# Performance work log

Measured on AMD Instinct MI355X. Metric: run time of the kernel, lower is better.

## Reference

```python
import jax, jax.numpy as jnp
import numpy as np

N_HEAD = 16


def _rope_tables(T, head_dim, dtype):
    # RotaryEmbedding buffers: freqs = outer(t, inv_freq), half-dim tables [T, head_dim//2]
    inv_freq = 1.0 / (10000.0 ** (jnp.arange(0, head_dim, 2, dtype=jnp.float32) / head_dim))
    freqs = jnp.arange(T, dtype=jnp.float32)[:, None] * inv_freq[None, :]
    return jnp.cos(freqs).astype(dtype), jnp.sin(freqs).astype(dtype)


def _apply_rotary(x, cos, sin):
    # x: [B,H,T,D]; cos/sin: [T,D//2] broadcast over B,H
    d = x.shape[-1] // 2
    x1, x2 = x[..., :d], x[..., d:]
    return jnp.concatenate([x1 * cos - x2 * sin, x2 * cos + x1 * sin], axis=-1)


def setup_inputs() -> dict:
    key = jax.random.key(0)
    k1, k2, k3 = jax.random.split(key, 3)
    B, T, C = 2, 2048, 2048
    x = jax.random.normal(k1, (B, T, C), dtype=jnp.float32)
    Wqkv = jax.random.normal(k2, (C, 3 * C), dtype=jnp.float32) * (1.0 / np.sqrt(C))
    Wproj = jax.random.normal(k3, (C, C), dtype=jnp.float32) * (1.0 / np.sqrt(C))
    return {"x": x, "Wqkv": Wqkv, "Wproj": Wproj}


def reference(x, Wqkv, Wproj):
    B, T, C = x.shape
    H = N_HEAD
    D = C // H
    qkv = (x @ Wqkv).reshape(B, T, 3, H, D)
    q, k, v = qkv[:, :, 0], qkv[:, :, 1], qkv[:, :, 2]  # [B,T,H,D]
    q = jnp.transpose(q, (0, 2, 1, 3))  # [B,H,T,D]
    k = jnp.transpose(k, (0, 2, 1, 3))
    v = jnp.transpose(v, (0, 2, 1, 3))
    cos, sin = _rope_tables(T, D, x.dtype)
    q = _apply_rotary(q, cos, sin)
    k = _apply_rotary(k, cos, sin)
    scale = 1.0 / np.sqrt(D)
    scores = jnp.einsum('bhqd,bhkd->bhqk', q, k) * scale
    causal = jnp.tril(jnp.ones((T, T), dtype=bool))
    scores = jnp.where(causal, scores, jnp.finfo(scores.dtype).min)
    attn = jax.nn.softmax(scores, axis=-1)
    out = jnp.einsum('bhqk,bhkd->bhqd', attn, v)
    out = jnp.transpose(out, (0, 2, 1, 3)).reshape(B, T, C)
    return out @ Wproj
```

## Files before the change

### kernel.cpp

```cpp
#include <hip/hip_runtime.h>
#include <hip/hip_bf16.h>

typedef short s16b;
using bf16x4 = __attribute__((ext_vector_type(4))) short;
using bf16x8 = __attribute__((ext_vector_type(8))) short;
using f32x4  = __attribute__((ext_vector_type(4))) float;
using u32x4  = __attribute__((ext_vector_type(4))) unsigned;

#define DEVINL __device__ __forceinline__

DEVINL float bf2f(short u) {
    union { float f; unsigned u; } x;
    x.u = ((unsigned)(unsigned short)u) << 16;
    return x.f;
}
DEVINL short f2bf(float f) {
    unsigned u = __builtin_bit_cast(unsigned, f);
    u += 0x7FFFu + ((u >> 16) & 1u);
    return (short)(u >> 16);
}
DEVINL unsigned cvtpk(float a, float b) {
    unsigned r;
    asm("v_cvt_pk_bf16_f32 %0, %1, %2" : "=v"(r) : "v"(a), "v"(b));
    return r;
}

DEVINL f32x4 mfma16(bf16x8 a, bf16x8 b, f32x4 c) {
    return __builtin_amdgcn_mfma_f32_16x16x32_bf16(a, b, c, 0, 0, 0);
}

DEVINL void gload_lds16(const void* g, void* lds_uniform) {
    __builtin_amdgcn_global_load_lds(
        (const __attribute__((address_space(1))) char*)(const char*)g,
        (__attribute__((address_space(3))) char*)(char*)lds_uniform, 16, 0, 0);
}

DEVINL int perm32(int k) {
    return ((k >> 2) & 3) * 8 + ((k >> 4) & 1) * 4 + (k & 3);
}

DEVINL bf16x8 lds256(const s16b* base, int row, int ds, int g) {
    const char* p = (const char*)base + row * 256 + ((((ds << 2) + g) ^ (row & 7)) << 4);
    return *(const bf16x8*)p;
}

__global__ void k_pre2(const float* __restrict__ x, s16b* __restrict__ xb,
                       float* __restrict__ ctab, float* __restrict__ stab,
                       const float* __restrict__ Wqkv, s16b* __restrict__ wqkvt,
                       const float* __restrict__ Wproj, s16b* __restrict__ wprojt) {
    __shared__ float tile[32][33];
    int bid = blockIdx.x;
    if (bid < 512) {
        int idx = bid * 256 + threadIdx.x;
        int i = idx & 63, t = idx >> 6;
        float inv = powf(10000.0f, -(float)i * (1.0f / 64.0f));
        float fr = (float)t * inv;
        ctab[idx] = cosf(fr);
        stab[idx] = sinf(fr);
    } else if (bid < 8704) {
        int idx = (bid - 512) * 256 + threadIdx.x;
        int p = idx * 4;
        int row = p >> 11, pc = p & 2047;
        int grp = pc >> 5, sp = pc & 31;
        int c = sp >> 3, half = (sp >> 2) & 1;
        int ksrc = grp * 32 + half * 16 + c * 4;
        float4 v = *(const float4*)(x + (size_t)row * 2048 + ksrc);
        bf16x4 o;
        o[0] = f2bf(v.x); o[1] = f2bf(v.y); o[2] = f2bf(v.z); o[3] = f2bf(v.w);
        *(bf16x4*)(xb + (size_t)row * 2048 + pc) = o;
    } else {
        int idx2 = bid - 8704;
        int bx = idx2 & 255, by = idx2 >> 8;
        const float* in; s16b* out; int C, c0;
        if (bx < 192) { in = Wqkv; out = wqkvt; C = 6144; c0 = bx * 32; }
        else          { in = Wproj; out = wprojt; C = 2048; c0 = (bx - 192) * 32; }
        int tx = threadIdx.x & 31, ty = threadIdx.x >> 5;
        int r0 = by * 32;
#pragma unroll
        for (int kk = 0; kk < 4; ++kk) {
            int r = ty + kk * 8;
            tile[r][tx] = in[(size_t)(r0 + r) * C + c0 + tx];
        }
        __syncthreads();
#pragma unroll
        for (int kk = 0; kk < 4; ++kk) {
            int r = ty + kk * 8;
            out[(size_t)(c0 + r) * 2048 + r0 + perm32(tx)] = f2bf(tile[tx][r]);
        }
    }
}

#define STG_B01(DB, KB)                                                        \
  gload_lds16(srcB + (KB), lds + 49152 + (DB) * 32768 + tid16);                \
  gload_lds16(srcB + 262144 + (KB), lds + 49152 + (DB) * 32768 + 8192 + tid16);
#define STG_B23(DB, KB)                                                        \
  gload_lds16(srcB + 524288 + (KB), lds + 49152 + (DB) * 32768 + 16384 + tid16); \
  gload_lds16(srcB + 786432 + (KB), lds + 49152 + (DB) * 32768 + 24576 + tid16);
#define STG_A01(DB, KB)                                                        \
  gload_lds16(srcA + (KB), lds + (DB) * 16384 + tid16);                        \
  gload_lds16(srcA + 262144 + (KB), lds + (DB) * 16384 + 8192 + tid16);

#define AF_READ(B, KS)                                                         \
    _Pragma("unroll")                                                          \
    for (int fi = 0; fi < 4; ++fi) {                                           \
      int row = (fi >> 1) * 64 + wm * 32 + (fi & 1) * 16 + r15;                \
      af[fi] = *(const bf16x8*)(lds + (B) * 16384 + row * 128                  \
               + ((((KS) * 4 + g) ^ (row & 7)) << 4));                         \
    }

#define PH4(B, KH, JH, STGC, WN)                                               \
  {                                                                            \
    if ((JH) == 0) { AF_READ(B, KH) }                                          \
    _Pragma("unroll")                                                          \
    for (int fj = 0; fj < 2; ++fj) {                                           \
      int row = (JH) * 128 + wn * 32 + fj * 16 + r15;                          \
      bfr[fj] = *(const bf16x8*)(lds + 49152 + (B) * 32768 + row * 128         \
                + ((((KH) * 4 + g) ^ (row & 7)) << 4));                        \
    }                                                                          \
    STGC                                                                       \
    if ((WN) == 6) { asm volatile("s_waitcnt vmcnt(6)" ::: "memory");          \
                     __builtin_amdgcn_sched_barrier(0); }                      \
    else if ((WN) == 0) { asm volatile("s_waitcnt vmcnt(0)" ::: "memory");     \
                     __builtin_amdgcn_sched_barrier(0); }                      \
    __builtin_amdgcn_s_barrier();                                              \
    asm volatile("s_waitcnt lgkmcnt(0)" ::: "memory");                         \
    __builtin_amdgcn_sched_barrier(0);                                         \
    __builtin_amdgcn_s_setprio(1);                                             \
    _Pragma("unroll")                                                          \
    for (int fi = 0; fi < 4; ++fi)                                             \
      _Pragma("unroll")                                                        \
      for (int fj = 0; fj < 2; ++fj)                                           \
        acc[fi][(JH) * 2 + fj] = mfma16(af[fi], bfr[fj], acc[fi][(JH) * 2 + fj]); \
    __builtin_amdgcn_s_setprio(0);                                             \
    __builtin_amdgcn_s_barrier();                                              \
    __builtin_amdgcn_sched_barrier(0);                                         \
  }

#define DO_TILE3(B, S1, S2, S3, WNL)                                           \
    PH4(B, 0, 0, S1, -1)                                                       \
    PH4(B, 0, 1, S2, -1)                                                       \
    PH4(B, 1, 0, S3, -1)                                                       \
    PH4(B, 1, 1, , WNL)

#define GEMM3_MAINLOOP(A_, B_)                                                 \
    __shared__ __attribute__((aligned(16))) char lds[147456];                  \
    const int tid = threadIdx.x;                                               \
    const int lane = tid & 63, wave = tid >> 6;                                \
    const int g = lane >> 4, r15 = lane & 15;                                  \
    const int wm = wave >> 2, wn = wave & 3;                                   \
    const int tid16 = tid << 4;                                                \
    const int rowL = tid16 >> 7;                                               \
    const int swzL = ((((tid16 >> 4) & 7) ^ (rowL & 7)) << 4);                 \
    const char* srcA = (const char*)(A_) + (size_t)(bm + rowL) * 4096 + swzL;  \
    const char* srcB = (const char*)(B_) + (size_t)(bn + rowL) * 4096 + swzL;  \
    f32x4 acc[4][4] = {};                                                      \
    bf16x8 af[4], bfr[2];                                                      \
    STG_B01(0, 0) STG_A01(0, 0) STG_B23(0, 0)                                  \
    STG_B01(1, 128) STG_A01(1, 128) STG_B23(1, 128)                            \
    asm volatile("s_waitcnt vmcnt(6)" ::: "memory");                           \
    __builtin_amdgcn_sched_barrier(0);                                         \
    __builtin_amdgcn_s_barrier();                                              \
    for (int t3 = 0; t3 < 10; ++t3) {                                          \
        const int kb2 = (3 * t3 + 2) * 128;                                    \
        const int kb3 = kb2 + 128, kb4 = kb2 + 256;                            \
        DO_TILE3(0, STG_B01(2, kb2), STG_A01(2, kb2), STG_B23(2, kb2), 6)      \
        DO_TILE3(1, STG_B01(0, kb3), STG_A01(0, kb3), STG_B23(0, kb3), 6)      \
        DO_TILE3(2, STG_B01(1, kb4), STG_A01(1, kb4), STG_B23(1, kb4), 6)      \
    }                                                                          \
    DO_TILE3(0, , , , 0)                                                       \
    DO_TILE3(1, , , , -1)

__global__ __launch_bounds__(512) void k_gemm_qkv(
    const s16b* __restrict__ A, const s16b* __restrict__ Bt,
    s16b* __restrict__ Qb, s16b* __restrict__ Kp, s16b* __restrict__ Vt,
    const float* __restrict__ ctab, const float* __restrict__ stab) {
    const int bid = blockIdx.x;
    const int xcd = bid & 7, local = bid >> 3;
    const int rr_ = local >> 5, w = local & 31;
    const int bm = ((xcd & 3) * 8 + (w >> 2)) * 128;
    const int bn = ((xcd >> 2) * 12 + rr_ * 4 + (w & 3)) * 256;
    GEMM3_MAINLOOP(A, Bt)
    const int which = bn >> 11;
    if (which < 2) {
        char* sml = (char*)lds;
#pragma unroll
        for (int i = 0; i < 4; ++i) {
#pragma unroll
            for (int j = 0; j < 4; ++j) {
                int mb0 = (i >> 1) * 64 + wm * 32 + (i & 1) * 16 + 4 * g;
                int nn = (j >> 1) * 128 + wn * 32 + (j & 1) * 16 + r15;
#pragma unroll
                for (int e = 0; e < 4; ++e) {
                    int mm = mb0 + e;
                    *(s16b*)(sml + mm * 528 + ((nn * 2) ^ ((mm & 3) << 5))) =
                        f2bf(acc[i][j][e]);
                }
            }
        }
        __syncthreads();
        const int mrow = tid >> 2, c4 = tid & 3;
        const int bb = bm >> 11;
        const int tt = (bm & 2047) + mrow;
        const char* srow = sml + mrow * 528;
        const int sw = (mrow & 3) << 5;
        bf16x8 v[8];
#pragma unroll
        for (int k = 0; k < 8; ++k) {
            int lc = c4 + 4 * k;
            v[k] = *(const bf16x8*)(srow + ((lc * 16) ^ sw));
        }
        float cs[2][8], sn[2][8];
#pragma unroll
        for (int j = 0; j < 2; ++j) {
            int d0 = 8 * c4 + 32 * j;
            const float* cp = ctab + tt * 64 + d0;
            const float* sp = stab + tt * 64 + d0;
            *(float4*)&cs[j][0] = *(const float4*)cp;
            *(float4*)&cs[j][4] = *(const float4*)(cp + 4);
            *(float4*)&sn[j][0] = *(const float4*)sp;
            *(float4*)&sn[j][4] = *(const float4*)(sp + 4);
        }
        if (which == 0) {
            const float SC = 0.12751744154f;
#pragma unroll
            for (int j = 0; j < 2; ++j)
#pragma unroll
                for (int e = 0; e < 8; ++e) { cs[j][e] *= SC; sn[j][e] *= SC; }
        }
        bf16x8 o[8];
#pragma unroll
        for (int hh = 0; hh < 2; ++hh)
#pragma unroll
            for (int j = 0; j < 2; ++j) {
                int kl = hh * 4 + j, kh = kl + 2;
                bf16x8 r1, r2;
#pragma unroll
                for (int e = 0; e < 8; ++e) {
                    float c = cs[j][e], s = sn[j][e];
                    float x1 = bf2f(v[kl][e]), x2 = bf2f(v[kh][e]);
                    r1[e] = f2bf(x1 * c - x2 * s);
                    r2[e] = f2bf(x2 * c + x1 * s);
                }
                o[kl] = r1; o[kh] = r2;
            }
        if (which == 0) {
#pragma unroll
            for (int k = 0; k < 8; ++k) {
                int lc = c4 + 4 * k;
                int ng = bn + lc * 8;
                int h = (ng >> 7) & 15, d = ng & 127;
                *(bf16x8*)(Qb + ((size_t)(bb * 16 + h) * 2048 + tt) * 128 + d) = o[k];
            }
        } else {
#pragma unroll
            for (int k = 0; k < 8; ++k) {
                int lc = c4 + 4 * k;
                int ng = bn + lc * 8;
                int h = (ng >> 7) & 15, d = ng & 127;
                size_t base = ((size_t)(bb * 16 + h) * 2048 + tt) * 128 + (d & ~31);
                int w2 = d & 31;
                bf16x4 lo, hi;
#pragma unroll
                for (int e = 0; e < 4; ++e) { lo[e] = o[k][e]; hi[e] = o[k][e + 4]; }
                *(bf16x4*)(Kp + base + perm32(w2)) = lo;
                *(bf16x4*)(Kp + base + perm32(w2 + 4)) = hi;
            }
        }
    } else {
#pragma unroll
        for (int i = 0; i < 4; ++i) {
            int m0 = bm + (i >> 1) * 64 + wm * 32 + (i & 1) * 16 + 4 * g;
            int b = m0 >> 11, t0 = m0 & 2047;
            int pt = (t0 & ~31) + perm32(t0 & 31);
#pragma unroll
            for (int j = 0; j < 4; ++j) {
                int n = bn + (j >> 1) * 128 + wn * 32 + (j & 1) * 16 + r15;
                int h = (n >> 7) & 15, d = n & 127;
                size_t base = ((size_t)(b * 16 + h) * 128 + d) * 2048 + pt;
                bf16x4 pk;
#pragma unroll
                for (int e = 0; e < 4; ++e) pk[e] = f2bf(acc[i][j][e]);
                *(bf16x4*)(Vt + base) = pk;
            }
        }
    }
}

__global__ __launch_bounds__(512) void k_gemm_proj(
    const s16b* __restrict__ A, const s16b* __restrict__ Bt, float* __restrict__ Co) {
    const int bid = blockIdx.x;
    const int xcd = bid & 7, local = bid >> 3;
    const int bm = (xcd * 4 + (local & 3)) * 128;
    const int bn = (local >> 2) * 256;
    GEMM3_MAINLOOP(A, Bt)
#pragma unroll
    for (int i = 0; i < 4; ++i) {
        int m0 = bm + (i >> 1) * 64 + wm * 32 + (i & 1) * 16 + 4 * g;
#pragma unroll
        for (int j = 0; j < 4; ++j) {
            int n = bn + (j >> 1) * 128 + wn * 32 + (j & 1) * 16 + r15;
#pragma unroll
            for (int e = 0; e < 4; ++e) Co[(size_t)(m0 + e) * 2048 + n] = acc[i][j][e];
        }
    }
}

__global__ __launch_bounds__(512) void k_attn(
    const s16b* __restrict__ Qb, const s16b* __restrict__ Kp,
    const s16b* __restrict__ Vt, s16b* __restrict__ AO) {
    __shared__ alignas(16) s16b Ks[2][128 * 128];
    __shared__ alignas(16) s16b Vs[2][128 * 128];
    const int tid = threadIdx.x;
    const int lane = tid & 63, wave = tid >> 6;
    const int g = lane >> 4, r15 = lane & 15;
    const int bh = blockIdx.x, pp = blockIdx.y;
    const s16b* Qg = Qb + (size_t)bh * 2048 * 128;
    const char* Kg = (const char*)(Kp + (size_t)bh * 2048 * 128);
    const char* Vg = (const char*)(Vt + (size_t)bh * 128 * 2048);
    const int b = bh >> 4, h = bh & 15;

#define ASTG(BUF, KT)                                                          \
    {                                                                          \
      const int k0s = (KT) * 128;                                              \
      _Pragma("unroll")                                                        \
      for (int rr = 0; rr < 4; ++rr) {                                         \
        int uo = (rr * 512 + wave * 64) * 16;                                  \
        int o = uo + lane * 16;                                                \
        int row = o >> 8, sl = (o >> 4) & 15;                                  \
        int sg = (sl ^ (row & 7)) << 4;                                        \
        gload_lds16(Kg + (size_t)(k0s + row) * 256 + sg,                       \
                    (char*)Ks + (BUF) * 32768 + uo);                           \
        gload_lds16(Vg + (size_t)row * 4096 + (size_t)k0s * 2 + sg,            \
                    (char*)Vs + (BUF) * 32768 + uo);                           \
      }                                                                        \
    }

    for (int pass = 0; pass < 2; ++pass) {
        const int qt = pass ? pp : (15 - pp);
        const int q0 = qt * 128 + wave * 16;
        const int ktiles = qt + 1;

        ASTG(0, 0)

        bf16x8 qf[4];
#pragma unroll
        for (int ds = 0; ds < 4; ++ds) {
            const s16b* p = Qg + (size_t)(q0 + r15) * 128 + ds * 32 + 4 * g;
            bf16x4 lo = *(const bf16x4*)p;
            bf16x4 hi = *(const bf16x4*)(p + 16);
            qf[ds] = __builtin_shufflevector(lo, hi, 0, 1, 2, 3, 4, 5, 6, 7);
        }

        f32x4 ot[8] = {};
        float m_s = -3e38f;
        float l_s = 0.f;

        for (int kt = 0; kt < ktiles; ++kt) {
            const int k0 = kt * 128;
            if (kt + 1 < ktiles) {
                ASTG((kt + 1) & 1, kt + 1)
                asm volatile("s_waitcnt vmcnt(8)" ::: "memory");
            } else {
                asm volatile("s_waitcnt vmcnt(0)" ::: "memory");
            }
            __builtin_amdgcn_sched_barrier(0);
            __builtin_amdgcn_s_barrier();
            asm volatile("" ::: "memory");
            __builtin_amdgcn_sched_barrier(0);

            if (k0 <= q0 + 15) {
                const s16b* Kb_ = (const s16b*)((const char*)Ks + (kt & 1) * 32768);
                const s16b* Vb_ = (const s16b*)((const char*)Vs + (kt & 1) * 32768);
                f32x4 st[8] = {};
                __builtin_amdgcn_s_setprio(1);
#pragma unroll
                for (int ds = 0; ds < 4; ++ds) {
#pragma unroll
                    for (int ks = 0; ks < 8; ++ks) {
                        bf16x8 kf = lds256(Kb_, ks * 16 + r15, ds, g);
                        st[ks] = mfma16(kf, qf[ds], st[ks]);
                    }
                }
                __builtin_amdgcn_s_setprio(0);
                if (k0 + 127 > q0) {
#pragma unroll
                    for (int ks = 0; ks < 8; ++ks)
#pragma unroll
                        for (int e = 0; e < 4; ++e) {
                            int kk = k0 + ks * 16 + 4 * g + e;
                            int qq = q0 + r15;
                            if (kk > qq) st[ks][e] = -3e38f;
                        }
                }
                {
                    float mx = st[0][0];
#pragma unroll
                    for (int ks = 0; ks < 8; ++ks)
#pragma unroll
                        for (int e = 0; e < 4; ++e)
                            if (ks | e) mx = fmaxf(mx, st[ks][e]);
                    mx = fmaxf(mx, __shfl_xor(mx, 16));
                    mx = fmaxf(mx, __shfl_xor(mx, 32));
                    if (__any(mx > m_s + 8.f)) {
                        float mn = fmaxf(m_s, mx);
                        float sf = exp2f(m_s - mn);
                        m_s = mn;
                        l_s *= sf;
#pragma unroll
                        for (int d8 = 0; d8 < 8; ++d8)
#pragma unroll
                            for (int e = 0; e < 4; ++e) ot[d8][e] *= sf;
                    }
                    float mm = m_s, sum = 0.f;
#pragma unroll
                    for (int ks = 0; ks < 8; ++ks)
#pragma unroll
                        for (int e = 0; e < 4; ++e) {
                            float p = exp2f(st[ks][e] - mm);
                            st[ks][e] = p;
                            sum += p;
                        }
                    l_s += sum;
                }
                bf16x8 pb[4];
#pragma unroll
                for (int k2 = 0; k2 < 4; ++k2) {
                    u32x4 t;
                    t[0] = cvtpk(st[2 * k2][0], st[2 * k2][1]);
                    t[1] = cvtpk(st[2 * k2][2], st[2 * k2][3]);
                    t[2] = cvtpk(st[2 * k2 + 1][0], st[2 * k2 + 1][1]);
                    t[3] = cvtpk(st[2 * k2 + 1][2], st[2 * k2 + 1][3]);
                    pb[k2] = __builtin_bit_cast(bf16x8, t);
                }
                __builtin_amdgcn_s_setprio(1);
#pragma unroll
                for (int k2 = 0; k2 < 4; ++k2)
#pragma unroll
                    for (int d8 = 0; d8 < 8; ++d8) {
                        bf16x8 vf = lds256(Vb_, d8 * 16 + r15, k2, g);
                        ot[d8] = mfma16(vf, pb[k2], ot[d8]);
                    }
                __builtin_amdgcn_s_setprio(0);
            }
            asm volatile("" ::: "memory");
            __builtin_amdgcn_sched_barrier(0);
            __builtin_amdgcn_s_barrier();
        }
        {
            float l = l_s;
            l += __shfl_xor(l, 16);
            l += __shfl_xor(l, 32);
            float inv = 1.0f / l;
            int q = q0 + r15;
#pragma unroll
            for (int d8 = 0; d8 < 8; ++d8) {
                uint2 pk2;
                pk2.x = cvtpk(ot[d8][0] * inv, ot[d8][1] * inv);
                pk2.y = cvtpk(ot[d8][2] * inv, ot[d8][3] * inv);
                size_t off = ((size_t)(b * 2048 + q)) * 2048
                           + h * 128 + (d8 >> 1) * 32 + g * 8 + (d8 & 1) * 4;
                *(uint2*)(AO + off) = pk2;
            }
        }
    }
#undef ASTG
}

extern "C" void kernel_launch(void* const* d_in, const int* in_sizes, int n_in,
                              void* d_out, int out_size, void* d_ws, size_t ws_size,
                              hipStream_t stream) {
    const float* x = (const float*)d_in[0];
    const float* Wqkv = (const float*)d_in[1];
    const float* Wproj = (const float*)d_in[2];
    float* out = (float*)d_out;

    char* ws = (char*)d_ws;
    float* ctab = (float*)ws;
    float* stab = ctab + 2048 * 64;
    size_t off = 1048576;
    s16b* xb = (s16b*)(ws + off); off += 16777216;
    s16b* wqkvt = (s16b*)(ws + off); off += 25165824;
    s16b* wprojt = (s16b*)(ws + off); off += 8388608;
    s16b* Qb = (s16b*)(ws + off); off += 16777216;
    s16b* Kp = (s16b*)(ws + off); off += 16777216;
    s16b* Vt = (s16b*)(ws + off); off += 16777216;
    s16b* AO = xb;

    k_pre2<<<dim3(25088), dim3(256), 0, stream>>>(x, xb, ctab, stab,
                                                  Wqkv, wqkvt, Wproj, wprojt);
    k_gemm_qkv<<<dim3(768), dim3(512), 0, stream>>>(xb, wqkvt, Qb, Kp, Vt, ctab, stab);
    k_attn<<<dim3(32, 8), dim3(512), 0, stream>>>(Qb, Kp, Vt, AO);
    k_gemm_proj<<<dim3(256), dim3(512), 0, stream>>>(AO, wprojt, out);
}
```

Measured before the change: 228.6 us.

## Switch GEMM kernels from 16x16x32 to 32x32x16 MFMA tiles

Rewrites the QKV and projection GEMM main loops to use 32x32x16 bf16 MFMA instructions with 2x2 accumulator tiles per wave instead of 4x4 16x16 tiles. The K-dimension permutation of the pre-packed operands (x, weights, and the attention output feeding the projection) changes to match the new MFMA operand layout, and the epilogues are rewritten for the 32x32 accumulator register mapping. The aim is fewer MFMA issues and LDS fragment reads per tile. The cost is a new register layout for the epilogue stores, which may be less coalesced, and fewer phases per K tile to overlap with loads.

```diff
diff --git a/kernel.cpp b/kernel.cpp
--- a/kernel.cpp
+++ b/kernel.cpp
@@ -5,6 +5,7 @@
 using bf16x4 = __attribute__((ext_vector_type(4))) short;
 using bf16x8 = __attribute__((ext_vector_type(8))) short;
 using f32x4  = __attribute__((ext_vector_type(4))) float;
+using f32x16 = __attribute__((ext_vector_type(16))) float;
 using u32x4  = __attribute__((ext_vector_type(4))) unsigned;
 
 #define DEVINL __device__ __forceinline__
@@ -28,6 +29,9 @@
 DEVINL f32x4 mfma16(bf16x8 a, bf16x8 b, f32x4 c) {
     return __builtin_amdgcn_mfma_f32_16x16x32_bf16(a, b, c, 0, 0, 0);
 }
+DEVINL f32x16 mfma32(bf16x8 a, bf16x8 b, f32x16 c) {
+    return __builtin_amdgcn_mfma_f32_32x32x16_bf16(a, b, c, 0, 0, 0);
+}
 
 DEVINL void gload_lds16(const void* g, void* lds_uniform) {
     __builtin_amdgcn_global_load_lds(
@@ -37,6 +41,10 @@
 
 DEVINL int perm32(int k) {
     return ((k >> 2) & 3) * 8 + ((k >> 4) & 1) * 4 + (k & 3);
+}
+DEVINL int perm16(int k) {
+    int c = (k >> 2) & 3;
+    return (k & ~15) | ((((c & 1) << 1) | (c >> 1)) << 2) | (k & 3);
 }
 
 DEVINL bf16x8 lds256(const s16b* base, int row, int ds, int g) {
@@ -61,9 +69,9 @@
         int idx = (bid - 512) * 256 + threadIdx.x;
         int p = idx * 4;
         int row = p >> 11, pc = p & 2047;
-        int grp = pc >> 5, sp = pc & 31;
-        int c = sp >> 3, half = (sp >> 2) & 1;
-        int ksrc = grp * 32 + half * 16 + c * 4;
+        int sc = (pc >> 2) & 3;
+        int csrc = ((sc & 1) << 1) | (sc >> 1);
+        int ksrc = (pc & ~15) + (csrc << 2);
         float4 v = *(const float4*)(x + (size_t)row * 2048 + ksrc);
         bf16x4 o;
         o[0] = f2bf(v.x); o[1] = f2bf(v.y); o[2] = f2bf(v.z); o[3] = f2bf(v.w);
@@ -85,7 +93,7 @@
 #pragma unroll
         for (int kk = 0; kk < 4; ++kk) {
             int r = ty + kk * 8;
-            out[(size_t)(c0 + r) * 2048 + r0 + perm32(tx)] = f2bf(tile[tx][r]);
+            out[(size_t)(c0 + r) * 2048 + r0 + perm16(tx)] = f2bf(tile[tx][r]);
         }
     }
 }
@@ -100,22 +108,23 @@
   gload_lds16(srcA + (KB), lds + (DB) * 16384 + tid16);                        \
   gload_lds16(srcA + 262144 + (KB), lds + (DB) * 16384 + 8192 + tid16);
 
-#define AF_READ(B, KS)                                                         \
+#define PH32(B, KS2, STGC, WN)                                                 \
+  {                                                                            \
     _Pragma("unroll")                                                          \
-    for (int fi = 0; fi < 4; ++fi) {                                           \
-      int row = (fi >> 1) * 64 + wm * 32 + (fi & 1) * 16 + r15;                \
-      af[fi] = *(const bf16x8*)(lds + (B) * 16384 + row * 128                  \
-               + ((((KS) * 4 + g) ^ (row & 7)) << 4));                         \
-    }
-
-#define PH4(B, KH, JH, STGC, WN)                                               \
-  {                                                                            \
-    if ((JH) == 0) { AF_READ(B, KH) }                                          \
-    _Pragma("unroll")                                                          \
-    for (int fj = 0; fj < 2; ++fj) {                                           \
-      int row = (JH) * 128 + wn * 32 + fj * 16 + r15;                          \
-      bfr[fj] = *(const bf16x8*)(lds + 49152 + (B) * 32768 + row * 128         \
-                + ((((KH) * 4 + g) ^ (row & 7)) << 4));                        \
+    for (int q = 0; q < 2; ++q) {                                              \
+      const int kk = (KS2) * 2 + q;                                            \
+      _Pragma("unroll")                                                        \
+      for (int mi = 0; mi < 2; ++mi) {                                         \
+        int row = wm * 64 + mi * 32 + l31;                                     \
+        af2[mi][q] = *(const bf16x8*)(lds + (B) * 16384 + row * 128            \
+                     + (((kk * 2 + hh5) ^ (row & 7)) << 4));                   \
+      }                                                                        \
+      _Pragma("unroll")                                                        \
+      for (int nj = 0; nj < 2; ++nj) {                                         \
+        int row = wn * 64 + nj * 32 + l31;                                     \
+        bf2[nj][q] = *(const bf16x8*)(lds + 49152 + (B) * 32768 + row * 128    \
+                     + (((kk * 2 + hh5) ^ (row & 7)) << 4));                   \
+      }                                                                        \
     }                                                                          \
     STGC                                                                       \
     if ((WN) == 6) { asm volatile("s_waitcnt vmcnt(6)" ::: "memory");          \
@@ -127,34 +136,34 @@
     __builtin_amdgcn_sched_barrier(0);                                         \
     __builtin_amdgcn_s_setprio(1);                                             \
     _Pragma("unroll")                                                          \
-    for (int fi = 0; fi < 4; ++fi)                                             \
+    for (int q = 0; q < 2; ++q)                                                \
       _Pragma("unroll")                                                        \
-      for (int fj = 0; fj < 2; ++fj)                                           \
-        acc[fi][(JH) * 2 + fj] = mfma16(af[fi], bfr[fj], acc[fi][(JH) * 2 + fj]); \
+      for (int mi = 0; mi < 2; ++mi)                                           \
+        _Pragma("unroll")                                                      \
+        for (int nj = 0; nj < 2; ++nj)                                         \
+          acc[mi][nj] = mfma32(af2[mi][q], bf2[nj][q], acc[mi][nj]);           \
     __builtin_amdgcn_s_setprio(0);                                             \
     __builtin_amdgcn_s_barrier();                                              \
     __builtin_amdgcn_sched_barrier(0);                                         \
   }
 
-#define DO_TILE3(B, S1, S2, S3, WNL)                                           \
-    PH4(B, 0, 0, S1, -1)                                                       \
-    PH4(B, 0, 1, S2, -1)                                                       \
-    PH4(B, 1, 0, S3, -1)                                                       \
-    PH4(B, 1, 1, , WNL)
-
-#define GEMM3_MAINLOOP(A_, B_)                                                 \
+#define DO_T32(B, S1, S2, S3, WNL)                                             \
+    PH32(B, 0, S1 S2, -1)                                                      \
+    PH32(B, 1, S3, WNL)
+
+#define GEMM32_MAINLOOP(A_, B_)                                                \
     __shared__ __attribute__((aligned(16))) char lds[147456];                  \
     const int tid = threadIdx.x;                                               \
     const int lane = tid & 63, wave = tid >> 6;                                \
-    const int g = lane >> 4, r15 = lane & 15;                                  \
+    const int l31 = lane & 31, hh5 = lane >> 5;                                \
     const int wm = wave >> 2, wn = wave & 3;                                   \
     const int tid16 = tid << 4;                                                \
     const int rowL = tid16 >> 7;                                               \
     const int swzL = ((((tid16 >> 4) & 7) ^ (rowL & 7)) << 4);                 \
     const char* srcA = (const char*)(A_) + (size_t)(bm + rowL) * 4096 + swzL;  \
     const char* srcB = (const char*)(B_) + (size_t)(bn + rowL) * 4096 + swzL;  \
-    f32x4 acc[4][4] = {};                                                      \
-    bf16x8 af[4], bfr[2];                                                      \
+    f32x16 acc[2][2] = {};                                                     \
+    bf16x8 af2[2][2], bf2[2][2];                                               \
     STG_B01(0, 0) STG_A01(0, 0) STG_B23(0, 0)                                  \
     STG_B01(1, 128) STG_A01(1, 128) STG_B23(1, 128)                            \
     asm volatile("s_waitcnt vmcnt(6)" ::: "memory");                           \
@@ -163,12 +172,12 @@
     for (int t3 = 0; t3 < 10; ++t3) {                                          \
         const int kb2 = (3 * t3 + 2) * 128;                                    \
         const int kb3 = kb2 + 128, kb4 = kb2 + 256;                            \
-        DO_TILE3(0, STG_B01(2, kb2), STG_A01(2, kb2), STG_B23(2, kb2), 6)      \
-        DO_TILE3(1, STG_B01(0, kb3), STG_A01(0, kb3), STG_B23(0, kb3), 6)      \
-        DO_TILE3(2, STG_B01(1, kb4), STG_A01(1, kb4), STG_B23(1, kb4), 6)      \
+        DO_T32(0, STG_B01(2, kb2), STG_A01(2, kb2), STG_B23(2, kb2), 6)        \
+        DO_T32(1, STG_B01(0, kb3), STG_A01(0, kb3), STG_B23(0, kb3), 6)        \
+        DO_T32(2, STG_B01(1, kb4), STG_A01(1, kb4), STG_B23(1, kb4), 6)        \
     }                                                                          \
-    DO_TILE3(0, , , , 0)                                                       \
-    DO_TILE3(1, , , , -1)
+    DO_T32(0, , , , 0)                                                         \
+    DO_T32(1, , , , -1)
 
 __global__ __launch_bounds__(512) void k_gemm_qkv(
     const s16b* __restrict__ A, const s16b* __restrict__ Bt,
@@ -179,24 +188,21 @@
     const int rr_ = local >> 5, w = local & 31;
     const int bm = ((xcd & 3) * 8 + (w >> 2)) * 128;
     const int bn = ((xcd >> 2) * 12 + rr_ * 4 + (w & 3)) * 256;
-    GEMM3_MAINLOOP(A, Bt)
+    GEMM32_MAINLOOP(A, Bt)
     const int which = bn >> 11;
     if (which < 2) {
         char* sml = (char*)lds;
 #pragma unroll
-        for (int i = 0; i < 4; ++i) {
-#pragma unroll
-            for (int j = 0; j < 4; ++j) {
-                int mb0 = (i >> 1) * 64 + wm * 32 + (i & 1) * 16 + 4 * g;
-                int nn = (j >> 1) * 128 + wn * 32 + (j & 1) * 16 + r15;
-#pragma unroll
-                for (int e = 0; e < 4; ++e) {
-                    int mm = mb0 + e;
+        for (int mi = 0; mi < 2; ++mi)
+#pragma unroll
+            for (int nj = 0; nj < 2; ++nj)
+#pragma unroll
+                for (int reg = 0; reg < 16; ++reg) {
+                    int mm = wm * 64 + mi * 32 + (reg & 3) + ((reg >> 2) << 3) + (hh5 << 2);
+                    int nn = wn * 64 + nj * 32 + l31;
                     *(s16b*)(sml + mm * 528 + ((nn * 2) ^ ((mm & 3) << 5))) =
-                        f2bf(acc[i][j][e]);
-                }
-            }
-        }
+                        f2bf(acc[mi][nj][reg]);
+                }
         __syncthreads();
         const int mrow = tid >> 2, c4 = tid & 3;
         const int bb = bm >> 11;
@@ -268,21 +274,22 @@
         }
     } else {
 #pragma unroll
-        for (int i = 0; i < 4; ++i) {
-            int m0 = bm + (i >> 1) * 64 + wm * 32 + (i & 1) * 16 + 4 * g;
-            int b = m0 >> 11, t0 = m0 & 2047;
-            int pt = (t0 & ~31) + perm32(t0 & 31);
-#pragma unroll
-            for (int j = 0; j < 4; ++j) {
-                int n = bn + (j >> 1) * 128 + wn * 32 + (j & 1) * 16 + r15;
-                int h = (n >> 7) & 15, d = n & 127;
-                size_t base = ((size_t)(b * 16 + h) * 128 + d) * 2048 + pt;
-                bf16x4 pk;
-#pragma unroll
-                for (int e = 0; e < 4; ++e) pk[e] = f2bf(acc[i][j][e]);
-                *(bf16x4*)(Vt + base) = pk;
-            }
-        }
+        for (int mi = 0; mi < 2; ++mi)
+#pragma unroll
+            for (int nj = 0; nj < 2; ++nj)
+#pragma unroll
+                for (int rq = 0; rq < 4; ++rq) {
+                    int m0 = bm + wm * 64 + mi * 32 + (rq << 3) + (hh5 << 2);
+                    int b = m0 >> 11, t0 = m0 & 2047;
+                    int pt = (t0 & ~31) + perm32(t0 & 31);
+                    int n = bn + wn * 64 + nj * 32 + l31;
+                    int h = (n >> 7) & 15, d = n & 127;
+                    size_t base = ((size_t)(b * 16 + h) * 128 + d) * 2048 + pt;
+                    bf16x4 pk;
+#pragma unroll
+                    for (int e = 0; e < 4; ++e) pk[e] = f2bf(acc[mi][nj][rq * 4 + e]);
+                    *(bf16x4*)(Vt + base) = pk;
+                }
     }
 }
 
@@ -292,17 +299,17 @@
     const int xcd = bid & 7, local = bid >> 3;
     const int bm = (xcd * 4 + (local & 3)) * 128;
     const int bn = (local >> 2) * 256;
-    GEMM3_MAINLOOP(A, Bt)
-#pragma unroll
-    for (int i = 0; i < 4; ++i) {
-        int m0 = bm + (i >> 1) * 64 + wm * 32 + (i & 1) * 16 + 4 * g;
-#pragma unroll
-        for (int j = 0; j < 4; ++j) {
-            int n = bn + (j >> 1) * 128 + wn * 32 + (j & 1) * 16 + r15;
-#pragma unroll
-            for (int e = 0; e < 4; ++e) Co[(size_t)(m0 + e) * 2048 + n] = acc[i][j][e];
-        }
-    }
+    GEMM32_MAINLOOP(A, Bt)
+#pragma unroll
+    for (int mi = 0; mi < 2; ++mi)
+#pragma unroll
+        for (int nj = 0; nj < 2; ++nj)
+#pragma unroll
+            for (int reg = 0; reg < 16; ++reg) {
+                int m = bm + wm * 64 + mi * 32 + (reg & 3) + ((reg >> 2) << 3) + (hh5 << 2);
+                int n = bn + wn * 64 + nj * 32 + l31;
+                Co[(size_t)m * 2048 + n] = acc[mi][nj][reg];
+            }
 }
 
 __global__ __launch_bounds__(512) void k_attn(
@@ -318,6 +325,7 @@
     const char* Kg = (const char*)(Kp + (size_t)bh * 2048 * 128);
     const char* Vg = (const char*)(Vt + (size_t)bh * 128 * 2048);
     const int b = bh >> 4, h = bh & 15;
+    const int swg = (((g & 1) << 1) | (g >> 1)) << 2;
 
 #define ASTG(BUF, KT)                                                          \
     {                                                                          \
@@ -458,7 +466,7 @@
                 pk2.x = cvtpk(ot[d8][0] * inv, ot[d8][1] * inv);
                 pk2.y = cvtpk(ot[d8][2] * inv, ot[d8][3] * inv);
                 size_t off = ((size_t)(b * 2048 + q)) * 2048
-                           + h * 128 + (d8 >> 1) * 32 + g * 8 + (d8 & 1) * 4;
+                           + h * 128 + d8 * 16 + swg;
                 *(uint2*)(AO + off) = pk2;
             }
         }
```

Result: slower. 248.1 us (+8.5%).

## Process both causal q-tiles concurrently with 32-row waves sharing K/V tiles

Applied to the files above, without the earlier changes.

Replaces the two sequential passes over paired query tiles (15-pp and pp) with a single pass. Waves 0-3 handle the long tile and waves 4-7 the short tile, each wave owning 32 query rows as two 16-row MFMA subtiles. Each K/V tile staged into LDS is loaded once and each LDS fragment read feeds two MFMAs, which halves LDS reads per FLOP and removes the second pass's reload of early K/V tiles. The cost is doubled accumulator and score registers, which may raise register pressure. Load imbalance also appears, since the short-tile waves sit idle at barriers for most iterations.

```diff
diff --git a/kernel.cpp b/kernel.cpp
--- a/kernel.cpp
+++ b/kernel.cpp
@@ -319,6 +319,11 @@
     const char* Vg = (const char*)(Vt + (size_t)bh * 128 * 2048);
     const int b = bh >> 4, h = bh & 15;
 
+    const int qt = (wave < 4) ? (15 - pp) : pp;
+    const int w2 = wave & 3;
+    const int q0 = qt * 128 + w2 * 32;
+    const int ktiles = 16 - pp;
+
 #define ASTG(BUF, KT)                                                          \
     {                                                                          \
       const int k0s = (KT) * 128;                                              \
@@ -335,132 +340,138 @@
       }                                                                        \
     }
 
-    for (int pass = 0; pass < 2; ++pass) {
-        const int qt = pass ? pp : (15 - pp);
-        const int q0 = qt * 128 + wave * 16;
-        const int ktiles = qt + 1;
-
-        ASTG(0, 0)
-
-        bf16x8 qf[4];
+    ASTG(0, 0)
+
+    bf16x8 qf[2][4];
+#pragma unroll
+    for (int qs = 0; qs < 2; ++qs)
 #pragma unroll
         for (int ds = 0; ds < 4; ++ds) {
-            const s16b* p = Qg + (size_t)(q0 + r15) * 128 + ds * 32 + 4 * g;
+            const s16b* p = Qg + (size_t)(q0 + qs * 16 + r15) * 128 + ds * 32 + 4 * g;
             bf16x4 lo = *(const bf16x4*)p;
             bf16x4 hi = *(const bf16x4*)(p + 16);
-            qf[ds] = __builtin_shufflevector(lo, hi, 0, 1, 2, 3, 4, 5, 6, 7);
-        }
-
-        f32x4 ot[8] = {};
-        float m_s = -3e38f;
-        float l_s = 0.f;
-
-        for (int kt = 0; kt < ktiles; ++kt) {
-            const int k0 = kt * 128;
-            if (kt + 1 < ktiles) {
-                ASTG((kt + 1) & 1, kt + 1)
-                asm volatile("s_waitcnt vmcnt(8)" ::: "memory");
-            } else {
-                asm volatile("s_waitcnt vmcnt(0)" ::: "memory");
-            }
-            __builtin_amdgcn_sched_barrier(0);
-            __builtin_amdgcn_s_barrier();
-            asm volatile("" ::: "memory");
-            __builtin_amdgcn_sched_barrier(0);
-
-            if (k0 <= q0 + 15) {
-                const s16b* Kb_ = (const s16b*)((const char*)Ks + (kt & 1) * 32768);
-                const s16b* Vb_ = (const s16b*)((const char*)Vs + (kt & 1) * 32768);
-                f32x4 st[8] = {};
-                __builtin_amdgcn_s_setprio(1);
-#pragma unroll
-                for (int ds = 0; ds < 4; ++ds) {
-#pragma unroll
-                    for (int ks = 0; ks < 8; ++ks) {
-                        bf16x8 kf = lds256(Kb_, ks * 16 + r15, ds, g);
-                        st[ks] = mfma16(kf, qf[ds], st[ks]);
-                    }
+            qf[qs][ds] = __builtin_shufflevector(lo, hi, 0, 1, 2, 3, 4, 5, 6, 7);
+        }
+
+    f32x4 ot[8][2] = {};
+    float m_s[2] = {-3e38f, -3e38f};
+    float l_s[2] = {0.f, 0.f};
+
+    for (int kt = 0; kt < ktiles; ++kt) {
+        const int k0 = kt * 128;
+        if (kt + 1 < ktiles) {
+            ASTG((kt + 1) & 1, kt + 1)
+            asm volatile("s_waitcnt vmcnt(8)" ::: "memory");
+        } else {
+            asm volatile("s_waitcnt vmcnt(0)" ::: "memory");
+        }
+        __builtin_amdgcn_sched_barrier(0);
+        __builtin_amdgcn_s_barrier();
+        asm volatile("" ::: "memory");
+        __builtin_amdgcn_sched_barrier(0);
+
+        if (k0 <= q0 + 31) {
+            const s16b* Kb_ = (const s16b*)((const char*)Ks + (kt & 1) * 32768);
+            const s16b* Vb_ = (const s16b*)((const char*)Vs + (kt & 1) * 32768);
+            f32x4 st[8][2] = {};
+            __builtin_amdgcn_s_setprio(1);
+#pragma unroll
+            for (int ds = 0; ds < 4; ++ds) {
+#pragma unroll
+                for (int ks = 0; ks < 8; ++ks) {
+                    bf16x8 kf = lds256(Kb_, ks * 16 + r15, ds, g);
+#pragma unroll
+                    for (int qs = 0; qs < 2; ++qs)
+                        st[ks][qs] = mfma16(kf, qf[qs][ds], st[ks][qs]);
                 }
-                __builtin_amdgcn_s_setprio(0);
-                if (k0 + 127 > q0) {
-#pragma unroll
-                    for (int ks = 0; ks < 8; ++ks)
+            }
+            __builtin_amdgcn_s_setprio(0);
+            if (k0 + 127 > q0) {
+#pragma unroll
+                for (int ks = 0; ks < 8; ++ks)
+#pragma unroll
+                    for (int qs = 0; qs < 2; ++qs)
 #pragma unroll
                         for (int e = 0; e < 4; ++e) {
                             int kk = k0 + ks * 16 + 4 * g + e;
-                            int qq = q0 + r15;
-                            if (kk > qq) st[ks][e] = -3e38f;
+                            int qq = q0 + qs * 16 + r15;
+                            if (kk > qq) st[ks][qs][e] = -3e38f;
                         }
+            }
+#pragma unroll
+            for (int qs = 0; qs < 2; ++qs) {
+                float mx = st[0][qs][0];
+#pragma unroll
+                for (int ks = 0; ks < 8; ++ks)
+#pragma unroll
+                    for (int e = 0; e < 4; ++e)
+                        if (ks | e) mx = fmaxf(mx, st[ks][qs][e]);
+                mx = fmaxf(mx, __shfl_xor(mx, 16));
+                mx = fmaxf(mx, __shfl_xor(mx, 32));
+                if (__any(mx > m_s[qs] + 8.f)) {
+                    float mn = fmaxf(m_s[qs], mx);
+                    float sf = exp2f(m_s[qs] - mn);
+                    m_s[qs] = mn;
+                    l_s[qs] *= sf;
+#pragma unroll
+                    for (int d8 = 0; d8 < 8; ++d8)
+#pragma unroll
+                        for (int e = 0; e < 4; ++e) ot[d8][qs][e] *= sf;
                 }
-                {
-                    float mx = st[0][0];
-#pragma unroll
-                    for (int ks = 0; ks < 8; ++ks)
-#pragma unroll
-                        for (int e = 0; e < 4; ++e)
-                            if (ks | e) mx = fmaxf(mx, st[ks][e]);
-                    mx = fmaxf(mx, __shfl_xor(mx, 16));
-                    mx = fmaxf(mx, __shfl_xor(mx, 32));
-                    if (__any(mx > m_s + 8.f)) {
-                        float mn = fmaxf(m_s, mx);
-                        float sf = exp2f(m_s - mn);
-                        m_s = mn;
-                        l_s *= sf;
-#pragma unroll
-                        for (int d8 = 0; d8 < 8; ++d8)
-#pragma unroll
-                            for (int e = 0; e < 4; ++e) ot[d8][e] *= sf;
+                float mm = m_s[qs], sum = 0.f;
+#pragma unroll
+                for (int ks = 0; ks < 8; ++ks)
+#pragma unroll
+                    for (int e = 0; e < 4; ++e) {
+                        float p = exp2f(st[ks][qs][e] - mm);
+                        st[ks][qs][e] = p;
+                        sum += p;
                     }
-                    float mm = m_s, sum = 0.f;
-#pragma unroll
-                    for (int ks = 0; ks < 8; ++ks)
-#pragma unroll
-                        for (int e = 0; e < 4; ++e) {
-                            float p = exp2f(st[ks][e] - mm);
-                            st[ks][e] = p;
-                            sum += p;
-                        }
-                    l_s += sum;
+                l_s[qs] += sum;
+            }
+            bf16x8 pb[4][2];
+#pragma unroll
+            for (int k2 = 0; k2 < 4; ++k2)
+#pragma unroll
+                for (int qs = 0; qs < 2; ++qs) {
+                    u32x4 t;
+                    t[0] = cvtpk(st[2 * k2][qs][0], st[2 * k2][qs][1]);
+                    t[1] = cvtpk(st[2 * k2][qs][2], st[2 * k2][qs][3]);
+                    t[2] = cvtpk(st[2 * k2 + 1][qs][0], st[2 * k2 + 1][qs][1]);
+                    t[3] = cvtpk(st[2 * k2 + 1][qs][2], st[2 * k2 + 1][qs][3]);
+                    pb[k2][qs] = __builtin_bit_cast(bf16x8, t);
                 }
-                bf16x8 pb[4];
-#pragma unroll
-                for (int k2 = 0; k2 < 4; ++k2) {
-                    u32x4 t;
-                    t[0] = cvtpk(st[2 * k2][0], st[2 * k2][1]);
-                    t[1] = cvtpk(st[2 * k2][2], st[2 * k2][3]);
-                    t[2] = cvtpk(st[2 * k2 + 1][0], st[2 * k2 + 1][1]);
-                    t[3] = cvtpk(st[2 * k2 + 1][2], st[2 * k2 + 1][3]);
-                    pb[k2] = __builtin_bit_cast(bf16x8, t);
+            __builtin_amdgcn_s_setprio(1);
+#pragma unroll
+            for (int k2 = 0; k2 < 4; ++k2)
+#pragma unroll
+                for (int d8 = 0; d8 < 8; ++d8) {
+                    bf16x8 vf = lds256(Vb_, d8 * 16 + r15, k2, g);
+#pragma unroll
+                    for (int qs = 0; qs < 2; ++qs)
+                        ot[d8][qs] = mfma16(vf, pb[k2][qs], ot[d8][qs]);
                 }
-                __builtin_amdgcn_s_setprio(1);
-#pragma unroll
-                for (int k2 = 0; k2 < 4; ++k2)
-#pragma unroll
-                    for (int d8 = 0; d8 < 8; ++d8) {
-                        bf16x8 vf = lds256(Vb_, d8 * 16 + r15, k2, g);
-                        ot[d8] = mfma16(vf, pb[k2], ot[d8]);
-                    }
-                __builtin_amdgcn_s_setprio(0);
-            }
-            asm volatile("" ::: "memory");
-            __builtin_amdgcn_sched_barrier(0);
-            __builtin_amdgcn_s_barrier();
-        }
-        {
-            float l = l_s;
-            l += __shfl_xor(l, 16);
-            l += __shfl_xor(l, 32);
-            float inv = 1.0f / l;
-            int q = q0 + r15;
-#pragma unroll
-            for (int d8 = 0; d8 < 8; ++d8) {
-                uint2 pk2;
-                pk2.x = cvtpk(ot[d8][0] * inv, ot[d8][1] * inv);
-                pk2.y = cvtpk(ot[d8][2] * inv, ot[d8][3] * inv);
-                size_t off = ((size_t)(b * 2048 + q)) * 2048
-                           + h * 128 + (d8 >> 1) * 32 + g * 8 + (d8 & 1) * 4;
-                *(uint2*)(AO + off) = pk2;
-            }
+            __builtin_amdgcn_s_setprio(0);
+        }
+        asm volatile("" ::: "memory");
+        __builtin_amdgcn_sched_barrier(0);
+        __builtin_amdgcn_s_barrier();
+    }
+#pragma unroll
+    for (int qs = 0; qs < 2; ++qs) {
+        float l = l_s[qs];
+        l += __shfl_xor(l, 16);
+        l += __shfl_xor(l, 32);
+        float inv = 1.0f / l;
+        int q = q0 + qs * 16 + r15;
+#pragma unroll
+        for (int d8 = 0; d8 < 8; ++d8) {
+            uint2 pk2;
+            pk2.x = cvtpk(ot[d8][qs][0] * inv, ot[d8][qs][1] * inv);
+            pk2.y = cvtpk(ot[d8][qs][2] * inv, ot[d8][qs][3] * inv);
+            size_t off = ((size_t)(b * 2048 + q)) * 2048
+                       + h * 128 + (d8 >> 1) * 32 + g * 8 + (d8 & 1) * 4;
+            *(uint2*)(AO + off) = pk2;
         }
     }
 #undef ASTG
```

Result: no change. 230.3 us (+0.7%).
